# Performance work log

Measured on AMD Instinct MI355X. Metric: run time of the kernel, lower is better.

Reference implementation:

```python
import jax, jax.numpy as jnp
import numpy as np

N_G, E_G = 50000, 800000
N_S, E_S = 10000, 160000
NF = 64
B = 8

def _w(key, shape):
    fan_in = shape[-1]
    return jax.random.normal(key, shape, dtype=jnp.float32) / np.sqrt(fan_in)

def setup_inputs() -> dict:
    key = jax.random.key(0)
    ks = jax.random.split(key, 40)
    inp = {
        "graph_x": jax.random.normal(ks[0], (N_G, NF), dtype=jnp.float32),
        "subgraph_x": jax.random.normal(ks[1], (N_S, NF), dtype=jnp.float32),
        "point": jax.random.normal(ks[2], (B, NF), dtype=jnp.float32),
        "graph_edge_index": jax.random.randint(ks[3], (2, E_G), 0, N_G),
        "graph_batch": jnp.sort(jax.random.randint(ks[4], (N_G,), 0, B)),
        "subgraph_edge_index": jax.random.randint(ks[5], (2, E_S), 0, N_S),
        "subgraph_batch": jnp.sort(jax.random.randint(ks[6], (N_S,), 0, B)),
    }
    # GraphConv params per branch: channel sizes 64->128->256->192
    dims = [(2 * NF, NF), (4 * NF, 2 * NF), (3 * NF, 4 * NF)]
    i = 7
    for pre in ("g", "s"):
        for li, (o, c) in enumerate(dims, start=1):
            inp[f"{pre}W{li}r"] = _w(ks[i], (o, c)); i += 1  # lin_rel (aggregated)
            inp[f"{pre}W{li}n"] = _w(ks[i], (o, c)); i += 1  # lin_root (self)
            inp[f"{pre}B{li}"] = jnp.zeros((o,), dtype=jnp.float32)
    inp["l1W"] = _w(ks[i], (600, 3 * NF + 3 * NF + NF)); i += 1
    inp["l1b"] = jnp.zeros((600,), dtype=jnp.float32)
    inp["l2W"] = _w(ks[i], (256, 600)); i += 1
    inp["l2b"] = jnp.zeros((256,), dtype=jnp.float32)
    inp["l3W"] = _w(ks[i], (NF, 256)); i += 1
    inp["l3b"] = jnp.zeros((NF,), dtype=jnp.float32)
    return inp

def _graph_conv(x, src, dst, Wr, Wn, b, n_nodes):
    # PyG GraphConv: out_i = Wr @ sum_{j->i} x_j + Wn @ x_i + b
    agg = jax.ops.segment_sum(x[src], dst, num_segments=n_nodes)
    return agg @ Wr.T + x @ Wn.T + b

def _scatter_mean(x, seg, num_segments):
    s = jax.ops.segment_sum(x, seg, num_segments=num_segments)
    cnt = jax.ops.segment_sum(jnp.ones((x.shape[0],), x.dtype), seg, num_segments=num_segments)
    return s / jnp.maximum(cnt, 1.0)[:, None]

def _branch(x, edge_index, batch, params, n_nodes):
    src, dst = edge_index[0], edge_index[1]
    for (Wr, Wn, b) in params:
        x = jax.nn.elu(_graph_conv(x, src, dst, Wr, Wn, b, n_nodes))
    return _scatter_mean(x, batch, B)

def reference(graph_x, subgraph_x, point,
              gW1r, gW1n, gB1, gW2r, gW2n, gB2, gW3r, gW3n, gB3,
              sW1r, sW1n, sB1, sW2r, sW2n, sB2, sW3r, sW3n, sB3,
              l1W, l1b, l2W, l2b, l3W, l3b,
              graph_edge_index, graph_batch, subgraph_edge_index, subgraph_batch):
    x1 = _branch(graph_x, graph_edge_index, graph_batch,
                 [(gW1r, gW1n, gB1), (gW2r, gW2n, gB2), (gW3r, gW3n, gB3)], N_G)
    x2 = _branch(subgraph_x, subgraph_edge_index, subgraph_batch,
                 [(sW1r, sW1n, sB1), (sW2r, sW2n, sB2), (sW3r, sW3n, sB3)], N_S)
    x = jnp.concatenate([x1, x2, point], axis=-1)  # [B, 448]
    x = jax.nn.relu(x @ l1W.T + l1b)
    x = jax.nn.relu(x @ l2W.T + l2b)
    return x @ l3W.T + l3b  # [B, 64]
```

## Files before the change

### kernel.cpp

```cpp
#include <hip/hip_runtime.h>
#include <cmath>

typedef __attribute__((ext_vector_type(8))) short short8;
typedef __attribute__((ext_vector_type(4))) float floatx4;
typedef __attribute__((ext_vector_type(2))) float floatx2;
typedef __attribute__((ext_vector_type(4))) int intx4;
typedef __attribute__((ext_vector_type(2))) int intx2;

#define N_G 50000
#define E_G 800000
#define N_S 10000
#define E_S 160000
#define NT (N_G + N_S)
#define ET (E_G + E_S)
#define BATCH 8
#define STRIDE 64
#define FPASS 8

__device__ __forceinline__ short f2b(float f) {
    unsigned u = __builtin_bit_cast(unsigned, f);
    u += 0x7FFF + ((u >> 16) & 1);
    return (short)(u >> 16);
}
__device__ __forceinline__ short8 fp8x8_to_bf16(intx2 w) {
    floatx2 f0 = __builtin_amdgcn_cvt_pk_f32_fp8(w[0], false);
    floatx2 f1 = __builtin_amdgcn_cvt_pk_f32_fp8(w[0], true);
    floatx2 f2 = __builtin_amdgcn_cvt_pk_f32_fp8(w[1], false);
    floatx2 f3 = __builtin_amdgcn_cvt_pk_f32_fp8(w[1], true);
    short8 r;
    r[0]=f2b(f0[0]); r[1]=f2b(f0[1]); r[2]=f2b(f1[0]); r[3]=f2b(f1[1]);
    r[4]=f2b(f2[0]); r[5]=f2b(f2[1]); r[6]=f2b(f3[0]); r[7]=f2b(f3[1]);
    return r;
}

struct RepArgs { const float* Wr[6]; const float* Wn[6]; short* dst[6]; int cin[6]; int nk[6]; int groups[6]; };
__global__ void init_kernel(const float* __restrict__ gx, const float* __restrict__ sx,
                            unsigned char* __restrict__ X0_8,
                            int* __restrict__ dcount, float* __restrict__ pooled,
                            const int* __restrict__ g_batch, const int* __restrict__ s_batch,
                            int* __restrict__ starts, RepArgs ra, int total_groups) {
    int t = blockIdx.x * blockDim.x + threadIdx.x;
    if (t < NT * 16) {
        size_t e = (size_t)t * 4;
        const float* src = (e < (size_t)N_G * 64) ? (gx + e) : (sx + (e - (size_t)N_G * 64));
        floatx4 v = *(const floatx4*)src;
        int w8 = 0;
        w8 = __builtin_amdgcn_cvt_pk_fp8_f32(v[0], v[1], w8, false);
        w8 = __builtin_amdgcn_cvt_pk_fp8_f32(v[2], v[3], w8, true);
        *(unsigned int*)(X0_8 + e) = (unsigned int)w8;
    }
    if (t < NT) dcount[t] = 0;
    if (t < 16 * 192) pooled[t] = 0.f;
    if (t <= 16) {
        int b = t;
        if (b == 16) { starts[16] = NT; }
        else {
            int key, n, base;
            const int* arr;
            if (b < 8) { arr = g_batch; n = N_G; key = b; base = 0; }
            else       { arr = s_batch; n = N_S; key = b - 8; base = N_G; }
            int lo = 0, hi = n;
            while (lo < hi) { int mid = (lo + hi) >> 1; if (arr[mid] < key) lo = mid + 1; else hi = mid; }
            starts[b] = base + lo;
        }
    }
    if (t < total_groups) {
        int seg = 0, off = t;
        while (seg < 5 && off >= ra.groups[seg]) { off -= ra.groups[seg]; ++seg; }
        int CIN = ra.cin[seg], NK = ra.nk[seg];
        int lane = off & 63;
        int rest = off >> 6;
        int tt = rest % NK;
        int ot = rest / NK;
        int o = ot * 16 + (lane & 15);
        int kk = tt * 32 + (lane >> 4) * 8;
        const float* src = (kk < CIN) ? (ra.Wr[seg] + (size_t)o * CIN + kk)
                                      : (ra.Wn[seg] + (size_t)o * CIN + (kk - CIN));
        floatx4 u0 = *(const floatx4*)src;
        floatx4 u1 = *(const floatx4*)(src + 4);
        short8 d;
        d[0]=f2b(u0[0]); d[1]=f2b(u0[1]); d[2]=f2b(u0[2]); d[3]=f2b(u0[3]);
        d[4]=f2b(u1[0]); d[5]=f2b(u1[1]); d[6]=f2b(u1[2]); d[7]=f2b(u1[3]);
        *(short8*)(ra.dst[seg] + (size_t)off * 8) = d;
    }
}

__global__ void fill_kernel(const int* __restrict__ g_ei, const int* __restrict__ s_ei,
                            int* __restrict__ dcount, int* __restrict__ csr) {
    int pass = blockIdx.x & (FPASS - 1);
    int lb   = blockIdx.x >> 3;
    int t = lb * blockDim.x + threadIdx.x;
    if (t >= ET) return;
    int dst;
    if (t < E_G) dst = g_ei[E_G + t];
    else         dst = s_ei[E_S + (t - E_G)] + N_G;
    int lo = pass * (NT / FPASS);
    int hi = lo + (NT / FPASS);
    if (dst < lo || dst >= hi) return;
    int src;
    if (t < E_G) src = g_ei[t];
    else         src = s_ei[t - E_G] + N_G;
    int slot = atomicAdd(&dcount[dst], 1);
    if (slot < STRIDE) csr[(size_t)dst * STRIDE + slot] = src;
}

template<int C>
__global__ void agg8_kernel(const unsigned char* __restrict__ x8, const int* __restrict__ dcount,
                            const int* __restrict__ csr, short* __restrict__ out) {
    constexpr int C16 = C / 16;
    int t = blockIdx.x * blockDim.x + threadIdx.x;
    if (t >= NT * C16) return;
    int node = t / C16;
    int ch   = t % C16;
    int e0 = node * STRIDE;
    int e1 = e0 + min(dcount[node], STRIDE);
    float acc[16];
    #pragma unroll
    for (int j = 0; j < 16; ++j) acc[j] = 0.f;
    for (int e = e0; e < e1; ++e) {
        int s = csr[e];
        intx4 w = *(const intx4*)(x8 + (size_t)s * C + ch * 16);
        #pragma unroll
        for (int q = 0; q < 4; ++q) {
            floatx2 f0 = __builtin_amdgcn_cvt_pk_f32_fp8(w[q], false);
            floatx2 f1 = __builtin_amdgcn_cvt_pk_f32_fp8(w[q], true);
            acc[q * 4 + 0] += f0[0];
            acc[q * 4 + 1] += f0[1];
            acc[q * 4 + 2] += f1[0];
            acc[q * 4 + 3] += f1[1];
        }
    }
    short8 o0, o1;
    #pragma unroll
    for (int j = 0; j < 8; ++j) { o0[j] = f2b(acc[j]); o1[j] = f2b(acc[8 + j]); }
    short8* q = (short8*)(out + (size_t)node * C + ch * 16);
    q[0] = o0; q[1] = o1;
}

template<int CIN, int COUT, int C, bool POOL>
__global__ __launch_bounds__(128, 5) void gemm_elu_kernel(
        const short* __restrict__ A1, const unsigned char* __restrict__ A2_8,
        const short* __restrict__ gWF, const short* __restrict__ sWF,
        const float* __restrict__ gB, const float* __restrict__ sB,
        unsigned char* __restrict__ out8,
        float* __restrict__ pooled, const int* __restrict__ starts) {
    constexpr int NK  = CIN / 16;
    constexpr int NOT = COUT / 16;
    constexpr int OTW = NOT / C;
    static_assert(NOT % C == 0, "C must divide NOT");
    constexpr int KH  = (NK > 8) ? 2 : 1;
    constexpr int NKH = NK / KH;
    constexpr int NTILE = NT / 16;
    constexpr int RG = NTILE / 2;
    constexpr int TSUB = N_G / 16;

    int rg8 = blockIdx.x & 7;
    int rest = blockIdx.x >> 3;
    int c = rest % C;
    int rg = (rest / C) * 8 + rg8;
    if (rg >= RG) return;

    int wid = threadIdx.x >> 6;
    int lane = threadIdx.x & 63;
    int id = lane & 15, quad = lane >> 4;
    int tile = rg * 2 + wid;
    bool sub = (tile >= TSUB);
    const short* WFl = sub ? sWF : gWF;
    const float* bias = sub ? sB : gB;
    int r0 = tile * 16;
    int arow = r0 + id;

    int seg0 = 0, seg1 = 0;
    if (POOL) {
        while (seg0 < 15 && starts[seg0 + 1] <= r0) ++seg0;
        seg1 = seg0;
        while (seg1 < 15 && starts[seg1 + 1] <= r0 + 15) ++seg1;
    }

    floatx4 acc[OTW];
    #pragma unroll
    for (int o = 0; o < OTW; ++o) acc[o] = floatx4{0.f, 0.f, 0.f, 0.f};

    for (int kh = 0; kh < KH; ++kh) {
        short8 a[NKH];
        #pragma unroll
        for (int t = 0; t < NKH; ++t) {
            int kk = (kh * NKH + t) * 32 + quad * 8;
            if (kk < CIN) {
                a[t] = *(const short8*)(A1 + (size_t)arow * CIN + kk);
            } else {
                intx2 w = *(const intx2*)(A2_8 + (size_t)arow * CIN + (kk - CIN));
                a[t] = fp8x8_to_bf16(w);
            }
        }
        #pragma unroll
        for (int otl = 0; otl < OTW; ++otl) {
            const short* wp = WFl + ((((size_t)(c * OTW + otl) * NK + kh * NKH) * 64) + lane) * 8;
            #pragma unroll
            for (int t = 0; t < NKH; ++t) {
                short8 b = *(const short8*)(wp + (size_t)t * 512);
                acc[otl] = __builtin_amdgcn_mfma_f32_16x16x32_bf16(a[t], b, acc[otl], 0, 0, 0);
            }
        }
    }

    #pragma unroll
    for (int otl = 0; otl < OTW; ++otl) {
        int o = (c * OTW + otl) * 16 + id;
        float bv = bias[o];
        float vr[4];
        #pragma unroll
        for (int rr = 0; rr < 4; ++rr) {
            float v = acc[otl][rr] + bv;
            vr[rr] = (v > 0.f) ? v : (__expf(v) - 1.f);
        }
        if (!POOL) {
            #pragma unroll
            for (int rr = 0; rr < 4; ++rr) {
                int nrow = r0 + quad * 4 + rr;
                int w8 = __builtin_amdgcn_cvt_pk_fp8_f32(vr[rr], vr[rr], 0, false);
                out8[(size_t)nrow * COUT + o] = (unsigned char)(w8 & 0xFF);
            }
        } else if (seg0 == seg1) {
            float vsum = vr[0] + vr[1] + vr[2] + vr[3];
            vsum += __shfl_down(vsum, 32, 64);
            vsum += __shfl_down(vsum, 16, 64);
            if (lane < 16) atomicAdd(&pooled[seg0 * 192 + o], vsum);
        } else {
            #pragma unroll
            for (int rr = 0; rr < 4; ++rr) {
                int nrow = r0 + quad * 4 + rr;
                int sg = seg0;
                while (sg < seg1 && starts[sg + 1] <= nrow) ++sg;
                atomicAdd(&pooled[sg * 192 + o], vr[rr]);
            }
        }
    }
}

__global__ __launch_bounds__(256) void mlp1_kernel(
        const float* __restrict__ pooled, const int* __restrict__ starts,
        const float* __restrict__ point, const float* __restrict__ W,
        const float* __restrict__ bias, float* __restrict__ out) {
    int wave = (blockIdx.x * blockDim.x + threadIdx.x) >> 6;
    int lane = threadIdx.x & 63;
    if (wave >= BATCH * 600) return;
    int b = wave / 600, o = wave % 600;
    float invg = 1.f / (float)max(starts[b + 1] - starts[b], 1);
    float invs = 1.f / (float)max(starts[9 + b] - starts[8 + b], 1);
    const float* w = W + (size_t)o * 448;
    float acc = 0.f;
    for (int i = lane; i < 448; i += 64) {
        float x;
        if (i < 192)      x = pooled[b * 192 + i] * invg;
        else if (i < 384) x = pooled[(8 + b) * 192 + (i - 192)] * invs;
        else              x = point[b * 64 + (i - 384)];
        acc += x * w[i];
    }
    #pragma unroll
    for (int off = 32; off > 0; off >>= 1) acc += __shfl_down(acc, off, 64);
    if (lane == 0) out[wave] = fmaxf(acc + bias[o], 0.f);
}

__global__ __launch_bounds__(256) void dense_wave_kernel(
        const float* __restrict__ in, const float* __restrict__ W,
        const float* __restrict__ bias, float* __restrict__ out,
        int I, int O, int relu) {
    int wave = (blockIdx.x * blockDim.x + threadIdx.x) >> 6;
    int lane = threadIdx.x & 63;
    if (wave >= BATCH * O) return;
    int b = wave / O, o = wave % O;
    const float* x = in + (size_t)b * I;
    const float* w = W + (size_t)o * I;
    float acc = 0.f;
    for (int i = lane; i < I; i += 64) acc += x[i] * w[i];
    #pragma unroll
    for (int off = 32; off > 0; off >>= 1) acc += __shfl_down(acc, off, 64);
    if (lane == 0) {
        acc += bias[o];
        if (relu) acc = fmaxf(acc, 0.f);
        out[wave] = acc;
    }
}

extern "C" void kernel_launch(void* const* d_in, const int* in_sizes, int n_in,
                              void* d_out, int out_size, void* d_ws, size_t ws_size,
                              hipStream_t stream) {
    const float* graph_x = (const float*)d_in[0];
    const float* sub_x   = (const float*)d_in[1];
    const float* point   = (const float*)d_in[2];
    const int*   g_ei    = (const int*)d_in[3];
    const int*   g_batch = (const int*)d_in[4];
    const int*   s_ei    = (const int*)d_in[5];
    const int*   s_batch = (const int*)d_in[6];
    const float* gB1=(const float*)d_in[9],  *gB2=(const float*)d_in[12], *gB3=(const float*)d_in[15];
    const float* sB1=(const float*)d_in[18], *sB2=(const float*)d_in[21], *sB3=(const float*)d_in[24];
    const float* l1W=(const float*)d_in[25], *l1b=(const float*)d_in[26];
    const float* l2W=(const float*)d_in[27], *l2b=(const float*)d_in[28];
    const float* l3W=(const float*)d_in[29], *l3b=(const float*)d_in[30];

    char* ws = (char*)d_ws;
    size_t off = 0;
    auto alloc = [&](size_t bytes) -> char* {
        char* p = ws + off;
        off = (off + bytes + 255) & ~(size_t)255;
        return p;
    };
    int* dcount = (int*)alloc((size_t)NT * 4);
    int* csr = (int*)alloc((size_t)NT * STRIDE * 4);

    const int fsz[3] = {128 * 2 * 64, 256 * 2 * 128, 192 * 2 * 256};
    short* wfrag = (short*)alloc((size_t)(fsz[0] + fsz[1] + fsz[2]) * 2 * 2);
    short* gWF[3], *sWF[3];
    { size_t o2 = 0;
      for (int l = 0; l < 3; ++l) { gWF[l] = wfrag + o2; o2 += fsz[l]; }
      for (int l = 0; l < 3; ++l) { sWF[l] = wfrag + o2; o2 += fsz[l]; } }

    unsigned char* X0_8 = (unsigned char*)alloc((size_t)NT * 64);
    short* agg = (short*)alloc((size_t)NT * 256 * 2);
    unsigned char* h1_8 = (unsigned char*)alloc((size_t)NT * 128);
    unsigned char* h2_8 = (unsigned char*)alloc((size_t)NT * 256);

    float* pooled = (float*)alloc(16 * 192 * 4);
    int* starts = (int*)alloc(17 * 4);
    float* mlp_h1 = (float*)alloc(BATCH * 600 * 4);
    float* mlp_h2 = (float*)alloc(BATCH * 256 * 4);

    RepArgs ra;
    const int cin_l[3] = {64, 128, 256};
    const int nk_l[3]  = {4, 8, 16};
    const int not_l[3] = {8, 16, 12};
    const int wr_idx[6] = {7, 10, 13, 16, 19, 22};
    int total_groups = 0;
    for (int s = 0; s < 6; ++s) {
        int l = s % 3;
        ra.Wr[s] = (const float*)d_in[wr_idx[s]];
        ra.Wn[s] = (const float*)d_in[wr_idx[s] + 1];
        ra.dst[s] = (s < 3) ? gWF[l] : sWF[l];
        ra.cin[s] = cin_l[l];
        ra.nk[s] = nk_l[l];
        ra.groups[s] = not_l[l] * nk_l[l] * 64;
        total_groups += ra.groups[s];
    }

    init_kernel<<<(NT * 16 + 255) / 256, 256, 0, stream>>>(graph_x, sub_x, X0_8, dcount,
                                                           pooled, g_batch, s_batch, starts,
                                                           ra, total_groups);

    fill_kernel<<<((ET + 255) / 256) * FPASS, 256, 0, stream>>>(g_ei, s_ei, dcount, csr);

    agg8_kernel<64><<<(NT * 4 + 255) / 256, 256, 0, stream>>>(X0_8, dcount, csr, agg);
    gemm_elu_kernel<64, 128, 2, false><<<235 * 2 * 8, 128, 0, stream>>>(
        agg, X0_8, gWF[0], sWF[0], gB1, sB1, h1_8, nullptr, nullptr);
    agg8_kernel<128><<<(NT * 8 + 255) / 256, 256, 0, stream>>>(h1_8, dcount, csr, agg);
    gemm_elu_kernel<128, 256, 4, false><<<235 * 4 * 8, 128, 0, stream>>>(
        agg, h1_8, gWF[1], sWF[1], gB2, sB2, h2_8, nullptr, nullptr);
    agg8_kernel<256><<<(NT * 16 + 255) / 256, 256, 0, stream>>>(h2_8, dcount, csr, agg);
    gemm_elu_kernel<256, 192, 4, true><<<235 * 4 * 8, 128, 0, stream>>>(
        agg, h2_8, gWF[2], sWF[2], gB3, sB3, nullptr, pooled, starts);

    mlp1_kernel<<<(BATCH * 600 + 3) / 4, 256, 0, stream>>>(pooled, starts, point, l1W, l1b, mlp_h1);
    dense_wave_kernel<<<(BATCH * 256 + 3) / 4, 256, 0, stream>>>(mlp_h1, l2W, l2b, mlp_h2, 600, 256, 1);
    dense_wave_kernel<<<(BATCH * 64 + 3) / 4, 256, 0, stream>>>(mlp_h2, l3W, l3b, (float*)d_out, 256, 64, 0);
}
```

Before: 393.2 us.

## Process two row tiles per wave and double-buffer weight fragments in GEMM

The GEMM+ELU kernel now has each wave compute two 16-row tiles, so every loaded weight fragment feeds two MFMAs. The full K extent of A is loaded up front, and B fragments are prefetched one output tile ahead when K is small. The grid is halved to match, and launch bounds drop from 5 to 2 waves per SIMD so the larger register footprint fits. The aim is to cut redundant weight loads and hide load latency, at the cost of lower occupancy and fewer, larger work units.

Result: no change. 394.8 us (+0.4%).

```diff
diff --git a/kernel.cpp b/kernel.cpp
--- a/kernel.cpp
+++ b/kernel.cpp
@@ -138,7 +138,7 @@
 }
 
 template<int CIN, int COUT, int C, bool POOL>
-__global__ __launch_bounds__(128, 5) void gemm_elu_kernel(
+__global__ __launch_bounds__(128, 2) void gemm_elu_kernel(
         const short* __restrict__ A1, const unsigned char* __restrict__ A2_8,
         const short* __restrict__ gWF, const short* __restrict__ sWF,
         const float* __restrict__ gB, const float* __restrict__ sB,
@@ -148,91 +148,138 @@
     constexpr int NOT = COUT / 16;
     constexpr int OTW = NOT / C;
     static_assert(NOT % C == 0, "C must divide NOT");
-    constexpr int KH  = (NK > 8) ? 2 : 1;
-    constexpr int NKH = NK / KH;
-    constexpr int NTILE = NT / 16;
-    constexpr int RG = NTILE / 2;
+    constexpr int NBUF = (NK <= 8) ? 2 : 1;
+    constexpr int MROW = 2;
     constexpr int TSUB = N_G / 16;
-
-    int rg8 = blockIdx.x & 7;
+    constexpr int TTOT = NT / 16;
+    constexpr int UG = (TSUB + MROW - 1) / MROW;
+    constexpr int US = (TTOT - TSUB + MROW - 1) / MROW;
+    constexpr int UTOT = UG + US;
+    constexpr int NBU = (UTOT + 1) / 2;
+
+    int bu8 = blockIdx.x & 7;
     int rest = blockIdx.x >> 3;
     int c = rest % C;
-    int rg = (rest / C) * 8 + rg8;
-    if (rg >= RG) return;
-
+    int bu = (rest / C) * 8 + bu8;
+    if (bu >= NBU) return;
     int wid = threadIdx.x >> 6;
+    int unit = bu * 2 + wid;
+    if (unit >= UTOT) return;
+
+    bool sub = (unit >= UG);
+    int t0, tmax;
+    if (!sub) { t0 = unit * MROW;                  tmax = TSUB - 1; }
+    else      { t0 = TSUB + (unit - UG) * MROW;    tmax = TTOT - 1; }
+    const short* WFl = sub ? sWF : gWF;
+    const float* bias = sub ? sB : gB;
+
     int lane = threadIdx.x & 63;
     int id = lane & 15, quad = lane >> 4;
-    int tile = rg * 2 + wid;
-    bool sub = (tile >= TSUB);
-    const short* WFl = sub ? sWF : gWF;
-    const float* bias = sub ? sB : gB;
-    int r0 = tile * 16;
-    int arow = r0 + id;
-
-    int seg0 = 0, seg1 = 0;
-    if (POOL) {
-        while (seg0 < 15 && starts[seg0 + 1] <= r0) ++seg0;
-        seg1 = seg0;
-        while (seg1 < 15 && starts[seg1 + 1] <= r0 + 15) ++seg1;
-    }
-
-    floatx4 acc[OTW];
-    #pragma unroll
-    for (int o = 0; o < OTW; ++o) acc[o] = floatx4{0.f, 0.f, 0.f, 0.f};
-
-    for (int kh = 0; kh < KH; ++kh) {
-        short8 a[NKH];
-        #pragma unroll
-        for (int t = 0; t < NKH; ++t) {
-            int kk = (kh * NKH + t) * 32 + quad * 8;
+
+    int tl[MROW]; bool act[MROW];
+    #pragma unroll
+    for (int m = 0; m < MROW; ++m) {
+        int t = t0 + m;
+        act[m] = (t <= tmax);
+        tl[m] = act[m] ? t : tmax;
+    }
+
+    short8 a[MROW][NK];
+    #pragma unroll
+    for (int m = 0; m < MROW; ++m) {
+        int arow = tl[m] * 16 + id;
+        #pragma unroll
+        for (int t = 0; t < NK; ++t) {
+            int kk = t * 32 + quad * 8;
             if (kk < CIN) {
-                a[t] = *(const short8*)(A1 + (size_t)arow * CIN + kk);
+                a[m][t] = *(const short8*)(A1 + (size_t)arow * CIN + kk);
             } else {
                 intx2 w = *(const intx2*)(A2_8 + (size_t)arow * CIN + (kk - CIN));
-                a[t] = fp8x8_to_bf16(w);
+                a[m][t] = fp8x8_to_bf16(w);
             }
         }
+    }
+
+    int seg0[MROW], seg1[MROW];
+    if (POOL) {
+        #pragma unroll
+        for (int m = 0; m < MROW; ++m) {
+            int r0 = tl[m] * 16;
+            int s0 = 0;
+            while (s0 < 15 && starts[s0 + 1] <= r0) ++s0;
+            int s1 = s0;
+            while (s1 < 15 && starts[s1 + 1] <= r0 + 15) ++s1;
+            seg0[m] = s0; seg1[m] = s1;
+        }
+    }
+
+    floatx4 acc[MROW][OTW];
+    #pragma unroll
+    for (int m = 0; m < MROW; ++m)
+        #pragma unroll
+        for (int o = 0; o < OTW; ++o) acc[m][o] = floatx4{0.f, 0.f, 0.f, 0.f};
+
+    auto bld = [&](int otl, int t) -> short8 {
+        return *(const short8*)(WFl + ((((size_t)(c * OTW + otl) * NK + t) * 64) + lane) * 8);
+    };
+
+    short8 bbuf[2][NK];
+    #pragma unroll
+    for (int t = 0; t < NK; ++t) bbuf[0][t] = bld(0, t);
+    #pragma unroll
+    for (int otl = 0; otl < OTW; ++otl) {
+        if (NBUF == 2) {
+            if (otl + 1 < OTW) {
+                #pragma unroll
+                for (int t = 0; t < NK; ++t) bbuf[(otl + 1) & 1][t] = bld(otl + 1, t);
+            }
+        } else if (otl > 0) {
+            #pragma unroll
+            for (int t = 0; t < NK; ++t) bbuf[0][t] = bld(otl, t);
+        }
+        const int rb = (NBUF == 2) ? (otl & 1) : 0;
+        #pragma unroll
+        for (int t = 0; t < NK; ++t) {
+            #pragma unroll
+            for (int m = 0; m < MROW; ++m)
+                acc[m][otl] = __builtin_amdgcn_mfma_f32_16x16x32_bf16(a[m][t], bbuf[rb][t], acc[m][otl], 0, 0, 0);
+        }
+    }
+
+    #pragma unroll
+    for (int m = 0; m < MROW; ++m) {
+        if (!act[m]) continue;
+        int r0 = tl[m] * 16;
         #pragma unroll
         for (int otl = 0; otl < OTW; ++otl) {
-            const short* wp = WFl + ((((size_t)(c * OTW + otl) * NK + kh * NKH) * 64) + lane) * 8;
-            #pragma unroll
-            for (int t = 0; t < NKH; ++t) {
-                short8 b = *(const short8*)(wp + (size_t)t * 512);
-                acc[otl] = __builtin_amdgcn_mfma_f32_16x16x32_bf16(a[t], b, acc[otl], 0, 0, 0);
-            }
-        }
-    }
-
-    #pragma unroll
-    for (int otl = 0; otl < OTW; ++otl) {
-        int o = (c * OTW + otl) * 16 + id;
-        float bv = bias[o];
-        float vr[4];
-        #pragma unroll
-        for (int rr = 0; rr < 4; ++rr) {
-            float v = acc[otl][rr] + bv;
-            vr[rr] = (v > 0.f) ? v : (__expf(v) - 1.f);
-        }
-        if (!POOL) {
+            int o = (c * OTW + otl) * 16 + id;
+            float bv = bias[o];
+            float vr[4];
             #pragma unroll
             for (int rr = 0; rr < 4; ++rr) {
-                int nrow = r0 + quad * 4 + rr;
-                int w8 = __builtin_amdgcn_cvt_pk_fp8_f32(vr[rr], vr[rr], 0, false);
-                out8[(size_t)nrow * COUT + o] = (unsigned char)(w8 & 0xFF);
+                float v = acc[m][otl][rr] + bv;
+                vr[rr] = (v > 0.f) ? v : (__expf(v) - 1.f);
             }
-        } else if (seg0 == seg1) {
-            float vsum = vr[0] + vr[1] + vr[2] + vr[3];
-            vsum += __shfl_down(vsum, 32, 64);
-            vsum += __shfl_down(vsum, 16, 64);
-            if (lane < 16) atomicAdd(&pooled[seg0 * 192 + o], vsum);
-        } else {
-            #pragma unroll
-            for (int rr = 0; rr < 4; ++rr) {
-                int nrow = r0 + quad * 4 + rr;
-                int sg = seg0;
-                while (sg < seg1 && starts[sg + 1] <= nrow) ++sg;
-                atomicAdd(&pooled[sg * 192 + o], vr[rr]);
+            if (!POOL) {
+                #pragma unroll
+                for (int rr = 0; rr < 4; ++rr) {
+                    int nrow = r0 + quad * 4 + rr;
+                    int w8 = __builtin_amdgcn_cvt_pk_fp8_f32(vr[rr], vr[rr], 0, false);
+                    out8[(size_t)nrow * COUT + o] = (unsigned char)(w8 & 0xFF);
+                }
+            } else if (seg0[m] == seg1[m]) {
+                float vsum = vr[0] + vr[1] + vr[2] + vr[3];
+                vsum += __shfl_down(vsum, 32, 64);
+                vsum += __shfl_down(vsum, 16, 64);
+                if (lane < 16) atomicAdd(&pooled[seg0[m] * 192 + o], vsum);
+            } else {
+                #pragma unroll
+                for (int rr = 0; rr < 4; ++rr) {
+                    int nrow = r0 + quad * 4 + rr;
+                    int sg = seg0[m];
+                    while (sg < seg1[m] && starts[sg + 1] <= nrow) ++sg;
+                    atomicAdd(&pooled[sg * 192 + o], vr[rr]);
+                }
             }
         }
     }
@@ -350,13 +397,13 @@
     fill_kernel<<<((ET + 255) / 256) * FPASS, 256, 0, stream>>>(g_ei, s_ei, dcount, csr);
 
     agg8_kernel<64><<<(NT * 4 + 255) / 256, 256, 0, stream>>>(X0_8, dcount, csr, agg);
-    gemm_elu_kernel<64, 128, 2, false><<<235 * 2 * 8, 128, 0, stream>>>(
+    gemm_elu_kernel<64, 128, 2, false><<<118 * 2 * 8, 128, 0, stream>>>(
         agg, X0_8, gWF[0], sWF[0], gB1, sB1, h1_8, nullptr, nullptr);
     agg8_kernel<128><<<(NT * 8 + 255) / 256, 256, 0, stream>>>(h1_8, dcount, csr, agg);
-    gemm_elu_kernel<128, 256, 4, false><<<235 * 4 * 8, 128, 0, stream>>>(
+    gemm_elu_kernel<128, 256, 4, false><<<118 * 4 * 8, 128, 0, stream>>>(
         agg, h1_8, gWF[1], sWF[1], gB2, sB2, h2_8, nullptr, nullptr);
     agg8_kernel<256><<<(NT * 16 + 255) / 256, 256, 0, stream>>>(h2_8, dcount, csr, agg);
-    gemm_elu_kernel<256, 192, 4, true><<<235 * 4 * 8, 128, 0, stream>>>(
+    gemm_elu_kernel<256, 192, 4, true><<<118 * 4 * 8, 128, 0, stream>>>(
         agg, h2_8, gWF[2], sWF[2], gB3, sB3, nullptr, pooled, starts);
 
     mlp1_kernel<<<(BATCH * 600 + 3) / 4, 256, 0, stream>>>(pooled, starts, point, l1W, l1b, mlp_h1);
```
